# Kernel optimization log

Hardware: AMD Instinct MI355X
Metric: run time of the kernel (lower is better)

Reference implementation:

```python
import jax, jax.numpy as jnp
import numpy as np

NEG = -1e30  # safe -inf surrogate (avoids nan grads through where)
NUM_CLASSES = 128
BLANK = NUM_CLASSES - 1
B, T, L = 256, 512, 64


def setup_inputs() -> dict:
    key = jax.random.key(0)
    k1, k2, k3, k4 = jax.random.split(key, 4)
    y_pred = jax.random.normal(k1, (B, T, NUM_CLASSES), dtype=jnp.float32)
    y_true = jax.random.randint(k2, (B, L), 0, BLANK, dtype=jnp.int32)  # labels in [0, C-2]
    input_length = jax.random.randint(k3, (B,), T // 2, T + 1, dtype=jnp.int32)
    label_length = jax.random.randint(k4, (B,), L // 2, L + 1, dtype=jnp.int32)
    return {"y_true": y_true, "y_pred": y_pred,
            "input_length": input_length, "label_length": label_length}


def ctc_loss(y_pred, y_true, input_length, label_length):
    # y_pred: [B,T,C] logits (batch-major), y_true: [B,L] int labels, blank = C-1.
    Bs, Ts, C = y_pred.shape
    Ls = y_true.shape[1]
    S = 2 * Ls + 1  # extended label lattice: blank, l1, blank, l2, ..., blank
    lp = jax.nn.log_softmax(y_pred.astype(jnp.float32), axis=-1)  # [B,T,C]
    z = jnp.full((Bs, S), BLANK, dtype=jnp.int32).at[:, 1::2].set(y_true)  # [B,S]
    idx = jnp.broadcast_to(z[:, None, :], (Bs, Ts, S))
    lp_z = jnp.take_along_axis(lp, idx, axis=2)  # [B,T,S] log p(z_s | t)
    # skip transition s-2 -> s allowed when z_s is a label differing from z_{s-2}
    s_idx = jnp.arange(S)
    z_m2 = jnp.pad(z[:, :-2], ((0, 0), (2, 0)), constant_values=BLANK)
    skip = (s_idx[None, :] >= 2) & (z != BLANK) & (z != z_m2)  # [B,S]
    alpha0 = (jnp.full((Bs, S), NEG, jnp.float32)
              .at[:, 0].set(lp_z[:, 0, 0])
              .at[:, 1].set(lp_z[:, 0, 1]))
    lps = jnp.moveaxis(lp_z[:, 1:, :], 1, 0)  # [T-1, B, S]
    ts = jnp.arange(1, Ts)

    def step(alpha, xs):
        t, lpt = xs
        a1 = jnp.pad(alpha[:, :-1], ((0, 0), (1, 0)), constant_values=NEG)
        a2 = jnp.where(skip, jnp.pad(alpha[:, :-2], ((0, 0), (2, 0)), constant_values=NEG), NEG)
        new = jnp.logaddexp(jnp.logaddexp(alpha, a1), a2) + lpt
        # freeze rows whose sequence already ended (t >= input_length)
        alpha = jnp.where((t < input_length)[:, None], new, alpha)
        return alpha, None

    alphaT, _ = jax.lax.scan(step, alpha0, (ts, lps))
    e1 = (2 * label_length)[:, None]  # final blank position per row
    a_end = jnp.take_along_axis(alphaT, e1, axis=1)[:, 0]
    a_end2 = jnp.take_along_axis(alphaT, e1 - 1, axis=1)[:, 0]
    return -jnp.logaddexp(a_end, a_end2)  # [B] negative log-likelihood


def reference(y_true, y_pred, input_length, label_length):
    # tf.nn.ctc_loss(labels, logits, label_length, logit_length,
    #                logits_time_major=False, blank_index=num_classes-1)
    return ctc_loss(y_pred, y_true, input_length, label_length)
```

## Files before the change

kernel.cpp:

```cpp
#include <hip/hip_runtime.h>
#include <hip/hip_fp16.h>
#include <math.h>


constexpr int Cc = 128;
constexpr int Tt = 512;
constexpr int Ll = 64;
constexpr int NPS = 7;
constexpr float INV_LN2 = 1.4426950408889634f;
constexpr float LN2_F   = 0.6931471805599453f;
constexpr float RENORM_THR = 16777216.0f;

__device__ __forceinline__ float fexp2(float x) { return __builtin_amdgcn_exp2f(x); }
__device__ __forceinline__ float flog2(float x) { return __builtin_amdgcn_logf(x); }

template<int CTRL, bool BC>
__device__ __forceinline__ float dppf(float old, float x) {
    return __int_as_float(__builtin_amdgcn_update_dpp(
        __float_as_int(old), __float_as_int(x), CTRL, 0xF, 0xF, BC));
}
__device__ __forceinline__ float wshr1(float x, float fill) { return dppf<0x138, false>(fill, x); }
__device__ __forceinline__ float wshl1(float x, float fill) { return dppf<0x130, false>(fill, x); }

__device__ __forceinline__ float rlf(float v, int lane) {
    return __int_as_float(__builtin_amdgcn_readlane(__float_as_int(v), lane));
}
__device__ __forceinline__ float rowsum(float e) {
    e += dppf<0x111, true>(0.f, e);
    e += dppf<0x112, true>(0.f, e);
    e += dppf<0x114, true>(0.f, e);
    e += dppf<0x118, true>(0.f, e);
    return e;
}
__device__ __forceinline__ float xmax64(float m) {
    m = fmaxf(m, __shfl_xor(m, 32, 64));
    m = fmaxf(m, __shfl_xor(m, 16, 64));
    m = fmaxf(m, __shfl_xor(m,  8, 64));
    m = fmaxf(m, __shfl_xor(m,  4, 64));
    m = fmaxf(m, __shfl_xor(m,  2, 64));
    m = fmaxf(m, __shfl_xor(m,  1, 64));
    return m;
}
__device__ __forceinline__ float bperm_f(int srclane, float v) {
    return __int_as_float(__builtin_amdgcn_ds_bpermute(srclane << 2, __float_as_int(v)));
}
__device__ __forceinline__ double shflx_d(double v, int mask) {
    const long long x = __double_as_longlong(v);
    int lo = (int)(x & 0xffffffffLL), hi = (int)(x >> 32);
    lo = __shfl_xor(lo, mask, 64);
    hi = __shfl_xor(hi, mask, 64);
    return __longlong_as_double(((long long)hi << 32) | (unsigned)(unsigned int)lo);
}

__device__ __forceinline__ void unpack8(uint4 raw, float (&dv)[8]) {
    const __half2 h0 = *reinterpret_cast<const __half2*>(&raw.x);
    const __half2 h1 = *reinterpret_cast<const __half2*>(&raw.y);
    const __half2 h2 = *reinterpret_cast<const __half2*>(&raw.z);
    const __half2 h3 = *reinterpret_cast<const __half2*>(&raw.w);
    dv[0] = __low2float(h0); dv[1] = __high2float(h0);
    dv[2] = __low2float(h1); dv[3] = __high2float(h1);
    dv[4] = __low2float(h2); dv[5] = __high2float(h2);
    dv[6] = __low2float(h3); dv[7] = __high2float(h3);
}

template<bool GUARD>
__device__ __forceinline__ void do_chunk(uint4 raw, int t0, int inlen, float skf,
                                         float& aO, float& aE, float& r0, float& Rtot)
{
    float dv[8]; unpack8(raw, dv);
    float sd[8];
#pragma unroll
    for (int j = 0; j < 8; ++j) sd[j] = skf * dv[j];
#pragma unroll
    for (int j = 0; j < 8; ++j) {
        if (!GUARD || (t0 + j < inlen)) {
            const float ad = aO * dv[j];
            const float pE = wshr1(aE, r0);
            const float pO = wshr1(aO, 0.0f);
            const float nO = fmaf(pE, dv[j], fmaf(pO, sd[j], ad));
            aE += aO;
            aO = nO;
        }
    }
    const float mx = fmaxf(fmaxf(aO, aE), r0);
    if (__any(mx >= RENORM_THR)) {
        const float M_ = xmax64(mx);
        int R_ = (int)(__float_as_uint(M_) >> 23) - 127;
        R_ = (R_ < 0) ? 0 : ((R_ > 126) ? 126 : R_);
        const float sc = __uint_as_float((unsigned)(127 - R_) << 23);
        aO = fminf(aO * sc, 4.0f);
        aE = fminf(aE * sc, 4.0f);
        r0 = fminf(r0 * sc, 4.0f);
        Rtot += (float)R_;
    }
}

template<bool GUARD>
__device__ __forceinline__ void do_chunk_bwd(uint4 raw, int t0, int inlen, float skfb,
                                             float& bO, float& bE, float& br, float& Rb,
                                             int l)
{
    float dv[8]; unpack8(raw, dv);
#pragma unroll
    for (int j = 7; j >= 0; --j) {
        if (!GUARD || (t0 + j < inlen)) {
            const float BOw = bO * dv[j];
            const float uO  = wshl1(BOw, 0.0f);
            const float t1  = bE + BOw;
            bE += uO;
            br += BOw;
            bO  = fmaf(skfb, uO, t1);
        }
    }
    const float brm = (l == 0) ? br : 0.0f;
    const float mx = fmaxf(fmaxf(bO, bE), brm);
    if (__any(mx >= RENORM_THR)) {
        const float M_ = xmax64(mx);
        int R_ = (int)(__float_as_uint(M_) >> 23) - 127;
        R_ = (R_ < 0) ? 0 : ((R_ > 126) ? 126 : R_);
        const float sc = __uint_as_float((unsigned)(127 - R_) << 23);
        bO = bO * sc;
        bE = bE * sc;
        br = br * sc;
        Rb += (float)R_;
    }
}

__global__ __launch_bounds__(1024, 1) void ctc_fused9_kernel(
    const int* __restrict__ y_true,
    const float* __restrict__ y_pred,
    const int* __restrict__ in_len,
    const int* __restrict__ lab_len,
    float* __restrict__ out)
{
    __shared__ __half w_lds[Tt / 8][64][8];
    __shared__ float  ps[2 * NPS];
    __shared__ int    fctr[10], bctr[10];
    __shared__ int    bdone, pdone;
    __shared__ float  bstate[130];

    const int b   = blockIdx.x;
    const int tid = threadIdx.x;
    const int w   = tid >> 6;
    const int l   = tid & 63;

    if (tid < 10) { fctr[tid] = 0; bctr[tid] = 0; }
    if (tid == 0) { bdone = 0; pdone = 0; }
    __syncthreads();

    int inlen = in_len[b]; if (inlen < 1) inlen = 1; if (inlen > Tt) inlen = Tt;
    int LLv   = lab_len[b]; if (LLv < 1) LLv = 1; if (LLv > Ll) LLv = Ll;

    const int nct  = (inlen + 7) >> 3;
    const int nchf = nct >> 1;
    const int nchb = nct - nchf;

    const int lab = y_true[b * Ll + l] & 127;
    const float* rowbase = y_pred + (size_t)b * Tt * Cc;

    if (w >= 2) {
        const bool asc = (w < 9);
        const int pw    = asc ? (w - 2) : (w - 9);
        const int nside = asc ? nchf : nchb;
        const int glane = lab >> 1;
        const int lsel  = lab & 1;
        const bool live = (l < LLv);
        int* ctr = asc ? fctr : bctr;

        float acc = 0.0f;

        for (int k = pw, idx = 0; k < nside; k += NPS, ++idx) {
            const int c = asc ? k : (nct - 1 - k);
            const int row0 = c * 8;
            float2 rv[8];
#pragma unroll
            for (int t = 0; t < 8; ++t)
                rv[t] = ((const float2*)(rowbase + (size_t)(row0 + t) * Cc))[l];

            float prod = 1.0f, bsum = 0.0f;
            uint4 pk;

            auto wbits = [&](int t) -> unsigned {
                const float2 v = rv[t];
                float e = fexp2(v.x * INV_LN2) + fexp2(v.y * INV_LN2);
                e = rowsum(e);
                const float s  = (rlf(e, 15) + rlf(e, 31)) + (rlf(e, 47) + rlf(e, 63));
                const float bl = rlf(v.y, 63);
                const bool ok = (row0 + t) < inlen;
                prod *= ok ? s : 1.0f;
                bsum += ok ? bl : 0.0f;
                const float xa = bperm_f(glane, v.x);
                const float xb = bperm_f(glane, v.y);
                const float xl = lsel ? xb : xa;
                float ww = fminf(fmaxf(fexp2((xl - bl) * INV_LN2), 6.1e-5f), 8192.0f);
                ww = live ? ww : 0.0f;
                return (unsigned)__half_as_ushort(__float2half(ww));
            };
            pk.x = wbits(0) | (wbits(1) << 16);
            pk.y = wbits(2) | (wbits(3) << 16);
            pk.z = wbits(4) | (wbits(5) << 16);
            pk.w = wbits(6) | (wbits(7) << 16);

            acc = fmaf(bsum, INV_LN2, acc) - flog2(prod);
            *(uint4*)&w_lds[c][l][0] = pk;
            asm volatile("s_waitcnt lgkmcnt(0)" ::: "memory");
            if (l == 0) atomicAdd(&ctr[idx], 1);
        }
        if (l == 0) ps[(asc ? 0 : NPS) + pw] = acc;
        asm volatile("s_waitcnt lgkmcnt(0)" ::: "memory");
        if (l == 0) atomicAdd(&pdone, 1);
        return;
    }

    const int labp = __shfl_up(lab, 1, 64);
    const float skf = ((l >= 1) && (lab != labp)) ? 1.0f : 0.0f;

    if (w == 1) {
        const float skfb = __shfl(skf, (l + 1) & 63, 64);
        float bE = (l == LLv - 1) ? 1.0f : 0.0f;
        float bO = bE;
        float br = 0.0f, Rb = 0.0f;

        volatile int* vd = bctr;
        int readyd = 0, rrd = 0;
        auto wait_d = [&](int cb) {
            const int needcnt = nct - cb;
            while (readyd < needcnt) {
                const int rem  = nchb - rrd * NPS;
                const int need = rem < NPS ? rem : NPS;
                if (vd[rrd] >= need) { readyd += need; ++rrd; }
                else __builtin_amdgcn_s_sleep(1);
            }
            asm volatile("" ::: "memory");
        };

        if (nchb > 0) {
            wait_d(nct - 1);
            uint4 A = *(const uint4*)&w_lds[nct - 1][l][0];
            for (int cb = nct - 1; cb >= nchf; --cb) {
                uint4 Bv = A;
                if (cb - 1 >= nchf) { wait_d(cb - 1); Bv = *(const uint4*)&w_lds[cb - 1][l][0]; }
                const int t0 = cb * 8;
                if (t0 + 8 <= inlen) do_chunk_bwd<false>(A, t0, inlen, skfb, bO, bE, br, Rb, l);
                else                 do_chunk_bwd<true >(A, t0, inlen, skfb, bO, bE, br, Rb, l);
                A = Bv;
            }
        }
        bstate[l]      = bE;
        bstate[64 + l] = bO;
        if (l == 0) { bstate[128] = br; bstate[129] = Rb; }
        asm volatile("s_waitcnt lgkmcnt(0)" ::: "memory");
        if (l == 0) atomicExch(&bdone, 1);
        return;
    }

    float aO = 0.0f, aE = 0.0f, r0 = 1.0f, Rf = 0.0f;

    volatile int* vf = fctr;
    int readyf = 0, rrf = 0;
    auto wait_f = [&](int cneed) {
        while (readyf <= cneed) {
            const int rem  = nchf - rrf * NPS;
            const int need = rem < NPS ? rem : NPS;
            if (vf[rrf] >= need) { readyf += need; ++rrf; }
            else __builtin_amdgcn_s_sleep(1);
        }
        asm volatile("" ::: "memory");
    };

    if (nchf > 0) {
        wait_f(0);
        uint4 A = *(const uint4*)&w_lds[0][l][0];
        for (int c = 0; c < nchf; ++c) {
            uint4 Bv = A;
            if (c + 1 < nchf) { wait_f(c + 1); Bv = *(const uint4*)&w_lds[c + 1][l][0]; }
            const int t0 = c * 8;
            if (t0 + 8 <= inlen) do_chunk<false>(A, t0, inlen, skf, aO, aE, r0, Rf);
            else                 do_chunk<true >(A, t0, inlen, skf, aO, aE, r0, Rf);
            A = Bv;
        }
    }

    {
        volatile int* vp = &pdone;
        while (*vp < 2 * NPS) __builtin_amdgcn_s_sleep(1);
        volatile int* vbd = &bdone;
        while (*vbd == 0) __builtin_amdgcn_s_sleep(1);
        asm volatile("" ::: "memory");
    }

    float cum_b = 0.0f;
#pragma unroll
    for (int q = 0; q < 2 * NPS; ++q) cum_b += ps[q];

    const float bEl = bstate[l], bOl = bstate[64 + l];
    const float br0 = bstate[128], Rb = bstate[129];
    double cd = (double)aE * (double)bEl + (double)aO * (double)bOl;
    if (l == 0) cd += (double)r0 * (double)br0;
#pragma unroll
    for (int mk = 1; mk < 64; mk <<= 1) cd += shflx_d(cd, mk);
    double sd_ = cd > 1e-300 ? cd : 1e-300;
    const long long u = __double_as_longlong(sd_);
    const int e2 = (int)((u >> 52) & 0x7ff) - 1023;
    const double mant = __longlong_as_double((u & 0xfffffffffffffLL) | 0x3ff0000000000000LL);
    const float l2s = (float)e2 + flog2((float)mant);
    if (l == 0)
        out[b] = -LN2_F * (l2s + Rf + Rb + cum_b);
}

extern "C" void kernel_launch(void* const* d_in, const int* in_sizes, int n_in,
                              void* d_out, int out_size, void* d_ws, size_t ws_size,
                              hipStream_t stream) {
    const int*   y_true  = (const int*)d_in[0];
    const float* y_pred  = (const float*)d_in[1];
    const int*   in_len  = (const int*)d_in[2];
    const int*   lab_len = (const int*)d_in[3];
    float*       out     = (float*)d_out;
    (void)d_ws; (void)ws_size;

    ctc_fused9_kernel<<<256, 1024, 0, stream>>>(y_true, y_pred, in_len, lab_len, out);
}
```

Baseline: 108.6 us.

## Decouple recurrence waves from normalizer waves; gather label logits directly with prefetch

Before, 14 producer waves computed per-timestep label weights, stored them to LDS as fp16, and signalled two recurrence waves through spin-waited counters. Now the forward and backward waves gather their own label logits and blank logits straight from global memory through a 4-deep register prefetch ring. The other waves only compute the log-sum-exp normalizer, using a DPP row-broadcast full-wave sum instead of four readlanes. A single __syncthreads replaces the flag polling. The intent is to remove the producer-consumer latency and the LDS traffic from the serial critical path, at the cost of scattered global gathers inside the recurrence waves. The forward path also drops its per-step inlen guard, and the launch bound changes to allow 4 blocks per CU.

```diff
diff --git a/kernel.cpp b/kernel.cpp
--- a/kernel.cpp
+++ b/kernel.cpp
@@ -6,7 +6,6 @@
 constexpr int Cc = 128;
 constexpr int Tt = 512;
 constexpr int Ll = 64;
-constexpr int NPS = 7;
 constexpr float INV_LN2 = 1.4426950408889634f;
 constexpr float LN2_F   = 0.6931471805599453f;
 constexpr float RENORM_THR = 16777216.0f;
@@ -30,6 +29,12 @@
     e += dppf<0x112, true>(0.f, e);
     e += dppf<0x114, true>(0.f, e);
     e += dppf<0x118, true>(0.f, e);
+    return e;
+}
+__device__ __forceinline__ float sum64_l63(float e) {
+    e = rowsum(e);
+    e += dppf<0x142, true>(0.f, e);
+    e += dppf<0x143, true>(0.f, e);
     return e;
 }
 __device__ __forceinline__ float xmax64(float m) {
@@ -41,9 +46,6 @@
     m = fmaxf(m, __shfl_xor(m,  1, 64));
     return m;
 }
-__device__ __forceinline__ float bperm_f(int srclane, float v) {
-    return __int_as_float(__builtin_amdgcn_ds_bpermute(srclane << 2, __float_as_int(v)));
-}
 __device__ __forceinline__ double shflx_d(double v, int mask) {
     const long long x = __double_as_longlong(v);
     int lo = (int)(x & 0xffffffffLL), hi = (int)(x >> 32);
@@ -52,35 +54,20 @@
     return __longlong_as_double(((long long)hi << 32) | (unsigned)(unsigned int)lo);
 }
 
-__device__ __forceinline__ void unpack8(uint4 raw, float (&dv)[8]) {
-    const __half2 h0 = *reinterpret_cast<const __half2*>(&raw.x);
-    const __half2 h1 = *reinterpret_cast<const __half2*>(&raw.y);
-    const __half2 h2 = *reinterpret_cast<const __half2*>(&raw.z);
-    const __half2 h3 = *reinterpret_cast<const __half2*>(&raw.w);
-    dv[0] = __low2float(h0); dv[1] = __high2float(h0);
-    dv[2] = __low2float(h1); dv[3] = __high2float(h1);
-    dv[4] = __low2float(h2); dv[5] = __high2float(h2);
-    dv[6] = __low2float(h3); dv[7] = __high2float(h3);
-}
-
-template<bool GUARD>
-__device__ __forceinline__ void do_chunk(uint4 raw, int t0, int inlen, float skf,
-                                         float& aO, float& aE, float& r0, float& Rtot)
+__device__ __forceinline__ void do_chunk_f(const float (&dv)[8], float skf,
+                                           float& aO, float& aE, float& r0, float& Rtot)
 {
-    float dv[8]; unpack8(raw, dv);
     float sd[8];
 #pragma unroll
     for (int j = 0; j < 8; ++j) sd[j] = skf * dv[j];
 #pragma unroll
     for (int j = 0; j < 8; ++j) {
-        if (!GUARD || (t0 + j < inlen)) {
-            const float ad = aO * dv[j];
-            const float pE = wshr1(aE, r0);
-            const float pO = wshr1(aO, 0.0f);
-            const float nO = fmaf(pE, dv[j], fmaf(pO, sd[j], ad));
-            aE += aO;
-            aO = nO;
-        }
+        const float ad = aO * dv[j];
+        const float pE = wshr1(aE, r0);
+        const float pO = wshr1(aO, 0.0f);
+        const float nO = fmaf(pE, dv[j], fmaf(pO, sd[j], ad));
+        aE += aO;
+        aO = nO;
     }
     const float mx = fmaxf(fmaxf(aO, aE), r0);
     if (__any(mx >= RENORM_THR)) {
@@ -96,11 +83,10 @@
 }
 
 template<bool GUARD>
-__device__ __forceinline__ void do_chunk_bwd(uint4 raw, int t0, int inlen, float skfb,
-                                             float& bO, float& bE, float& br, float& Rb,
-                                             int l)
+__device__ __forceinline__ void do_chunk_b(const float (&dv)[8], int t0, int inlen,
+                                           float skfb, float& bO, float& bE,
+                                           float& br, float& Rb, int l)
 {
-    float dv[8]; unpack8(raw, dv);
 #pragma unroll
     for (int j = 7; j >= 0; --j) {
         if (!GUARD || (t0 + j < inlen)) {
@@ -126,28 +112,21 @@
     }
 }
 
-__global__ __launch_bounds__(1024, 1) void ctc_fused9_kernel(
+__global__ __launch_bounds__(1024, 4) void ctc_fused11_kernel(
     const int* __restrict__ y_true,
     const float* __restrict__ y_pred,
     const int* __restrict__ in_len,
     const int* __restrict__ lab_len,
     float* __restrict__ out)
 {
-    __shared__ __half w_lds[Tt / 8][64][8];
-    __shared__ float  ps[2 * NPS];
-    __shared__ int    fctr[10], bctr[10];
-    __shared__ int    bdone, pdone;
-    __shared__ float  bstate[130];
+    __shared__ float ps[14];
+    __shared__ float bstate[130];
 
     const int b   = blockIdx.x;
     const int tid = threadIdx.x;
     const int w   = tid >> 6;
     const int l   = tid & 63;
 
-    if (tid < 10) { fctr[tid] = 0; bctr[tid] = 0; }
-    if (tid == 0) { bdone = 0; pdone = 0; }
-    __syncthreads();
-
     int inlen = in_len[b]; if (inlen < 1) inlen = 1; if (inlen > Tt) inlen = Tt;
     int LLv   = lab_len[b]; if (LLv < 1) LLv = 1; if (LLv > Ll) LLv = Ll;
 
@@ -158,154 +137,143 @@
     const int lab = y_true[b * Ll + l] & 127;
     const float* rowbase = y_pred + (size_t)b * Tt * Cc;
 
+    const int labp = __shfl_up(lab, 1, 64);
+    const float skf = ((l >= 1) && (lab != labp)) ? 1.0f : 0.0f;
+    const bool live = (l < LLv);
+
     if (w >= 2) {
-        const bool asc = (w < 9);
-        const int pw    = asc ? (w - 2) : (w - 9);
-        const int nside = asc ? nchf : nchb;
-        const int glane = lab >> 1;
-        const int lsel  = lab & 1;
-        const bool live = (l < LLv);
-        int* ctr = asc ? fctr : bctr;
-
+        const int wv = w - 2;
         float acc = 0.0f;
-
-        for (int k = pw, idx = 0; k < nside; k += NPS, ++idx) {
-            const int c = asc ? k : (nct - 1 - k);
-            const int row0 = c * 8;
-            float2 rv[8];
-#pragma unroll
-            for (int t = 0; t < 8; ++t)
-                rv[t] = ((const float2*)(rowbase + (size_t)(row0 + t) * Cc))[l];
-
+        float2 A[4], Bb[4];
+        auto loadg = [&](int g, float2 (&buf)[4]) {
+#pragma unroll
+            for (int q = 0; q < 4; ++q) {
+                const int r  = wv * 4 + q + 56 * g;
+                const int rc = (r < inlen) ? r : 0;
+                buf[q] = ((const float2*)(rowbase + (size_t)rc * Cc))[l];
+            }
+        };
+        auto procg = [&](int g, float2 (&buf)[4]) {
             float prod = 1.0f, bsum = 0.0f;
-            uint4 pk;
-
-            auto wbits = [&](int t) -> unsigned {
-                const float2 v = rv[t];
+#pragma unroll
+            for (int q = 0; q < 4; ++q) {
+                const float2 v = buf[q];
+                {
+                    const int r  = wv * 4 + q + 56 * (g + 2);
+                    const int rc = (r < inlen) ? r : 0;
+                    buf[q] = ((const float2*)(rowbase + (size_t)rc * Cc))[l];
+                }
+                const int r = wv * 4 + q + 56 * g;
                 float e = fexp2(v.x * INV_LN2) + fexp2(v.y * INV_LN2);
-                e = rowsum(e);
-                const float s  = (rlf(e, 15) + rlf(e, 31)) + (rlf(e, 47) + rlf(e, 63));
+                e = sum64_l63(e);
+                const float s  = rlf(e, 63);
                 const float bl = rlf(v.y, 63);
-                const bool ok = (row0 + t) < inlen;
+                const bool ok = r < inlen;
                 prod *= ok ? s : 1.0f;
                 bsum += ok ? bl : 0.0f;
-                const float xa = bperm_f(glane, v.x);
-                const float xb = bperm_f(glane, v.y);
-                const float xl = lsel ? xb : xa;
-                float ww = fminf(fmaxf(fexp2((xl - bl) * INV_LN2), 6.1e-5f), 8192.0f);
-                ww = live ? ww : 0.0f;
-                return (unsigned)__half_as_ushort(__float2half(ww));
-            };
-            pk.x = wbits(0) | (wbits(1) << 16);
-            pk.y = wbits(2) | (wbits(3) << 16);
-            pk.z = wbits(4) | (wbits(5) << 16);
-            pk.w = wbits(6) | (wbits(7) << 16);
-
+            }
             acc = fmaf(bsum, INV_LN2, acc) - flog2(prod);
-            *(uint4*)&w_lds[c][l][0] = pk;
-            asm volatile("s_waitcnt lgkmcnt(0)" ::: "memory");
-            if (l == 0) atomicAdd(&ctr[idx], 1);
-        }
-        if (l == 0) ps[(asc ? 0 : NPS) + pw] = acc;
-        asm volatile("s_waitcnt lgkmcnt(0)" ::: "memory");
-        if (l == 0) atomicAdd(&pdone, 1);
-        return;
-    }
-
-    const int labp = __shfl_up(lab, 1, 64);
-    const float skf = ((l >= 1) && (lab != labp)) ? 1.0f : 0.0f;
-
-    if (w == 1) {
+        };
+        loadg(0, A); loadg(1, Bb);
+        for (int g = 0; g < 10; g += 2) { procg(g, A); procg(g + 1, Bb); }
+        if (l == 0) ps[wv] = acc;
+    } else if (w == 1) {
         const float skfb = __shfl(skf, (l + 1) & 63, 64);
         float bE = (l == LLv - 1) ? 1.0f : 0.0f;
         float bO = bE;
         float br = 0.0f, Rb = 0.0f;
-
-        volatile int* vd = bctr;
-        int readyd = 0, rrd = 0;
-        auto wait_d = [&](int cb) {
-            const int needcnt = nct - cb;
-            while (readyd < needcnt) {
-                const int rem  = nchb - rrd * NPS;
-                const int need = rem < NPS ? rem : NPS;
-                if (vd[rrd] >= need) { readyd += need; ++rrd; }
-                else __builtin_amdgcn_s_sleep(1);
-            }
-            asm volatile("" ::: "memory");
-        };
-
-        if (nchb > 0) {
-            wait_d(nct - 1);
-            uint4 A = *(const uint4*)&w_lds[nct - 1][l][0];
-            for (int cb = nct - 1; cb >= nchf; --cb) {
-                uint4 Bv = A;
-                if (cb - 1 >= nchf) { wait_d(cb - 1); Bv = *(const uint4*)&w_lds[cb - 1][l][0]; }
-                const int t0 = cb * 8;
-                if (t0 + 8 <= inlen) do_chunk_bwd<false>(A, t0, inlen, skfb, bO, bE, br, Rb, l);
-                else                 do_chunk_bwd<true >(A, t0, inlen, skfb, bO, bE, br, Rb, l);
-                A = Bv;
-            }
+        const int nch = nchb;
+
+        float X0[8], X1[8], X2[8], X3[8];
+        float V0, V1, V2, V3;
+        auto issue = [&](int k, float (&X)[8], float& BV) {
+            const int cc = (k < nch) ? k : (nch - 1);
+            const int row0 = (nct - 1 - cc) * 8;
+#pragma unroll
+            for (int j = 0; j < 8; ++j)
+                X[j] = rowbase[(size_t)(row0 + j) * Cc + lab];
+            BV = rowbase[(size_t)(row0 + (l & 7)) * Cc + 127];
+        };
+        auto compute = [&](int k, float (&X)[8], float& BV) {
+            if (k >= nch) return;
+            float dv[8];
+#pragma unroll
+            for (int j = 0; j < 8; ++j) {
+                const float bl = __shfl(BV, j, 64);
+                const float ww = fminf(fmaxf(fexp2((X[j] - bl) * INV_LN2),
+                                             6.1e-5f), 8192.0f);
+                dv[j] = live ? ww : 0.0f;
+            }
+            const int t0 = (nct - 1 - k) * 8;
+            if (t0 + 8 <= inlen) do_chunk_b<false>(dv, t0, inlen, skfb, bO, bE, br, Rb, l);
+            else                 do_chunk_b<true >(dv, t0, inlen, skfb, bO, bE, br, Rb, l);
+        };
+        issue(0, X0, V0); issue(1, X1, V1); issue(2, X2, V2);
+        for (int k = 0; k < nch; k += 4) {
+            issue(k + 3, X3, V3); compute(k + 0, X0, V0);
+            issue(k + 4, X0, V0); compute(k + 1, X1, V1);
+            issue(k + 5, X1, V1); compute(k + 2, X2, V2);
+            issue(k + 6, X2, V2); compute(k + 3, X3, V3);
         }
         bstate[l]      = bE;
         bstate[64 + l] = bO;
         if (l == 0) { bstate[128] = br; bstate[129] = Rb; }
-        asm volatile("s_waitcnt lgkmcnt(0)" ::: "memory");
-        if (l == 0) atomicExch(&bdone, 1);
-        return;
-    }
-
+    }
     float aO = 0.0f, aE = 0.0f, r0 = 1.0f, Rf = 0.0f;
-
-    volatile int* vf = fctr;
-    int readyf = 0, rrf = 0;
-    auto wait_f = [&](int cneed) {
-        while (readyf <= cneed) {
-            const int rem  = nchf - rrf * NPS;
-            const int need = rem < NPS ? rem : NPS;
-            if (vf[rrf] >= need) { readyf += need; ++rrf; }
-            else __builtin_amdgcn_s_sleep(1);
+    if (w == 0) {
+        const int nch = nchf;
+        float X0[8], X1[8], X2[8], X3[8];
+        float V0, V1, V2, V3;
+        auto issue = [&](int k, float (&X)[8], float& BV) {
+            const int cc = (k < nch) ? k : (nch - 1);
+            const int row0 = cc * 8;
+#pragma unroll
+            for (int j = 0; j < 8; ++j)
+                X[j] = rowbase[(size_t)(row0 + j) * Cc + lab];
+            BV = rowbase[(size_t)(row0 + (l & 7)) * Cc + 127];
+        };
+        auto compute = [&](int k, float (&X)[8], float& BV) {
+            if (k >= nch) return;
+            float dv[8];
+#pragma unroll
+            for (int j = 0; j < 8; ++j) {
+                const float bl = __shfl(BV, j, 64);
+                const float ww = fminf(fmaxf(fexp2((X[j] - bl) * INV_LN2),
+                                             6.1e-5f), 8192.0f);
+                dv[j] = live ? ww : 0.0f;
+            }
+            do_chunk_f(dv, skf, aO, aE, r0, Rf);
+        };
+        issue(0, X0, V0); issue(1, X1, V1); issue(2, X2, V2);
+        for (int k = 0; k < nch; k += 4) {
+            issue(k + 3, X3, V3); compute(k + 0, X0, V0);
+            issue(k + 4, X0, V0); compute(k + 1, X1, V1);
+            issue(k + 5, X1, V1); compute(k + 2, X2, V2);
+            issue(k + 6, X2, V2); compute(k + 3, X3, V3);
         }
-        asm volatile("" ::: "memory");
-    };
-
-    if (nchf > 0) {
-        wait_f(0);
-        uint4 A = *(const uint4*)&w_lds[0][l][0];
-        for (int c = 0; c < nchf; ++c) {
-            uint4 Bv = A;
-            if (c + 1 < nchf) { wait_f(c + 1); Bv = *(const uint4*)&w_lds[c + 1][l][0]; }
-            const int t0 = c * 8;
-            if (t0 + 8 <= inlen) do_chunk<false>(A, t0, inlen, skf, aO, aE, r0, Rf);
-            else                 do_chunk<true >(A, t0, inlen, skf, aO, aE, r0, Rf);
-            A = Bv;
-        }
-    }
-
-    {
-        volatile int* vp = &pdone;
-        while (*vp < 2 * NPS) __builtin_amdgcn_s_sleep(1);
-        volatile int* vbd = &bdone;
-        while (*vbd == 0) __builtin_amdgcn_s_sleep(1);
-        asm volatile("" ::: "memory");
-    }
-
-    float cum_b = 0.0f;
-#pragma unroll
-    for (int q = 0; q < 2 * NPS; ++q) cum_b += ps[q];
-
-    const float bEl = bstate[l], bOl = bstate[64 + l];
-    const float br0 = bstate[128], Rb = bstate[129];
-    double cd = (double)aE * (double)bEl + (double)aO * (double)bOl;
-    if (l == 0) cd += (double)r0 * (double)br0;
-#pragma unroll
-    for (int mk = 1; mk < 64; mk <<= 1) cd += shflx_d(cd, mk);
-    double sd_ = cd > 1e-300 ? cd : 1e-300;
-    const long long u = __double_as_longlong(sd_);
-    const int e2 = (int)((u >> 52) & 0x7ff) - 1023;
-    const double mant = __longlong_as_double((u & 0xfffffffffffffLL) | 0x3ff0000000000000LL);
-    const float l2s = (float)e2 + flog2((float)mant);
-    if (l == 0)
-        out[b] = -LN2_F * (l2s + Rf + Rb + cum_b);
+    }
+
+    __syncthreads();
+
+    if (w == 0) {
+        float cum_b = 0.0f;
+#pragma unroll
+        for (int q = 0; q < 14; ++q) cum_b += ps[q];
+
+        const float bEl = bstate[l], bOl = bstate[64 + l];
+        const float br0 = bstate[128], Rb = bstate[129];
+        double cd = (double)aE * (double)bEl + (double)aO * (double)bOl;
+        if (l == 0) cd += (double)r0 * (double)br0;
+#pragma unroll
+        for (int mk = 1; mk < 64; mk <<= 1) cd += shflx_d(cd, mk);
+        double sd_ = cd > 1e-300 ? cd : 1e-300;
+        const long long u = __double_as_longlong(sd_);
+        const int e2 = (int)((u >> 52) & 0x7ff) - 1023;
+        const double mant = __longlong_as_double((u & 0xfffffffffffffLL) | 0x3ff0000000000000LL);
+        const float l2s = (float)e2 + flog2((float)mant);
+        if (l == 0)
+            out[b] = -LN2_F * (l2s + Rf + Rb + cum_b);
+    }
 }
 
 extern "C" void kernel_launch(void* const* d_in, const int* in_sizes, int n_in,
@@ -318,5 +286,5 @@
     float*       out     = (float*)d_out;
     (void)d_ws; (void)ws_size;
 
-    ctc_fused9_kernel<<<256, 1024, 0, stream>>>(y_true, y_pred, in_len, lab_len, out);
-}
+    ctc_fused11_kernel<<<256, 1024, 0, stream>>>(y_true, y_pred, in_len, lab_len, out);
+}
```

Result: slower. 114.9 us (+5.8%).

## Split forward and backward CTC passes into separate blocks with combine kernel

Applied to the files above, without the earlier changes.

Launches two blocks per batch row, one running the forward alpha recursion and one the backward beta recursion, each with 15 producer waves computing emission weights into LDS. A small second kernel combines the two halves' states from workspace memory into the final loss. This is meant to double block-level parallelism and give each serial recursion more producer waves. In exchange it adds a second launch and a global-memory round trip, and it keeps the old single-block kernel as a fallback when no workspace is available.

```diff
diff --git a/kernel.cpp b/kernel.cpp
--- a/kernel.cpp
+++ b/kernel.cpp
@@ -6,10 +6,10 @@
 constexpr int Cc = 128;
 constexpr int Tt = 512;
 constexpr int Ll = 64;
-constexpr int NPS = 7;
 constexpr float INV_LN2 = 1.4426950408889634f;
 constexpr float LN2_F   = 0.6931471805599453f;
 constexpr float RENORM_THR = 16777216.0f;
+constexpr int PAYSTRIDE = 132;
 
 __device__ __forceinline__ float fexp2(float x) { return __builtin_amdgcn_exp2f(x); }
 __device__ __forceinline__ float flog2(float x) { return __builtin_amdgcn_logf(x); }
@@ -63,9 +63,8 @@
     dv[6] = __low2float(h3); dv[7] = __high2float(h3);
 }
 
-template<bool GUARD>
-__device__ __forceinline__ void do_chunk(uint4 raw, int t0, int inlen, float skf,
-                                         float& aO, float& aE, float& r0, float& Rtot)
+__device__ __forceinline__ void do_chunk_f(uint4 raw, float skf,
+                                           float& aO, float& aE, float& r0, float& Rtot)
 {
     float dv[8]; unpack8(raw, dv);
     float sd[8];
@@ -73,14 +72,12 @@
     for (int j = 0; j < 8; ++j) sd[j] = skf * dv[j];
 #pragma unroll
     for (int j = 0; j < 8; ++j) {
-        if (!GUARD || (t0 + j < inlen)) {
-            const float ad = aO * dv[j];
-            const float pE = wshr1(aE, r0);
-            const float pO = wshr1(aO, 0.0f);
-            const float nO = fmaf(pE, dv[j], fmaf(pO, sd[j], ad));
-            aE += aO;
-            aO = nO;
-        }
+        const float ad = aO * dv[j];
+        const float pE = wshr1(aE, r0);
+        const float pO = wshr1(aO, 0.0f);
+        const float nO = fmaf(pE, dv[j], fmaf(pO, sd[j], ad));
+        aE += aO;
+        aO = nO;
     }
     const float mx = fmaxf(fmaxf(aO, aE), r0);
     if (__any(mx >= RENORM_THR)) {
@@ -96,9 +93,9 @@
 }
 
 template<bool GUARD>
-__device__ __forceinline__ void do_chunk_bwd(uint4 raw, int t0, int inlen, float skfb,
-                                             float& bO, float& bE, float& br, float& Rb,
-                                             int l)
+__device__ __forceinline__ void do_chunk_b(uint4 raw, int t0, int inlen, float skfb,
+                                           float& bO, float& bE, float& br, float& Rb,
+                                           int l)
 {
     float dv[8]; unpack8(raw, dv);
 #pragma unroll
@@ -126,51 +123,53 @@
     }
 }
 
-__global__ __launch_bounds__(1024, 1) void ctc_fused9_kernel(
+__global__ __launch_bounds__(1024, 8) void ctc_half_kernel(
     const int* __restrict__ y_true,
     const float* __restrict__ y_pred,
     const int* __restrict__ in_len,
     const int* __restrict__ lab_len,
-    float* __restrict__ out)
+    float* __restrict__ pay)
 {
-    __shared__ __half w_lds[Tt / 8][64][8];
-    __shared__ float  ps[2 * NPS];
-    __shared__ int    fctr[10], bctr[10];
-    __shared__ int    bdone, pdone;
-    __shared__ float  bstate[130];
-
-    const int b   = blockIdx.x;
+    constexpr int NPSH = 15;
+    constexpr int NRDH = 3;
+    __shared__ __half w_lds[32][64][8];
+    __shared__ float  ps[NPSH];
+    __shared__ int    ctr[NRDH];
+
+    const int dir = blockIdx.x & 1;
+    const int b   = blockIdx.x >> 1;
     const int tid = threadIdx.x;
     const int w   = tid >> 6;
     const int l   = tid & 63;
 
-    if (tid < 10) { fctr[tid] = 0; bctr[tid] = 0; }
-    if (tid == 0) { bdone = 0; pdone = 0; }
+    if (tid < NRDH) ctr[tid] = 0;
     __syncthreads();
 
     int inlen = in_len[b]; if (inlen < 1) inlen = 1; if (inlen > Tt) inlen = Tt;
     int LLv   = lab_len[b]; if (LLv < 1) LLv = 1; if (LLv > Ll) LLv = Ll;
 
-    const int nct  = (inlen + 7) >> 3;
-    const int nchf = nct >> 1;
-    const int nchb = nct - nchf;
+    const int nct   = (inlen + 7) >> 3;
+    const int nchf  = nct >> 1;
+    const int nchb  = nct - nchf;
+    const int nside = dir ? nchb : nchf;
 
     const int lab = y_true[b * Ll + l] & 127;
     const float* rowbase = y_pred + (size_t)b * Tt * Cc;
 
-    if (w >= 2) {
-        const bool asc = (w < 9);
-        const int pw    = asc ? (w - 2) : (w - 9);
-        const int nside = asc ? nchf : nchb;
+    const int labp = __shfl_up(lab, 1, 64);
+    const float skf = ((l >= 1) && (lab != labp)) ? 1.0f : 0.0f;
+    const bool live = (l < LLv);
+
+    float stE = 0.0f, stO = 0.0f, stX = 0.0f, stR = 0.0f;
+
+    if (w >= 1) {
+        const int pw = w - 1;
         const int glane = lab >> 1;
         const int lsel  = lab & 1;
-        const bool live = (l < LLv);
-        int* ctr = asc ? fctr : bctr;
-
         float acc = 0.0f;
 
-        for (int k = pw, idx = 0; k < nside; k += NPS, ++idx) {
-            const int c = asc ? k : (nct - 1 - k);
+        for (int k = pw, idx = 0; k < nside; k += NPSH, ++idx) {
+            const int c = dir ? (nct - 1 - k) : k;
             const int row0 = c * 8;
             float2 rv[8];
 #pragma unroll
@@ -179,7 +178,6 @@
 
             float prod = 1.0f, bsum = 0.0f;
             uint4 pk;
-
             auto wbits = [&](int t) -> unsigned {
                 const float2 v = rv[t];
                 float e = fexp2(v.x * INV_LN2) + fexp2(v.y * INV_LN2);
@@ -202,6 +200,167 @@
             pk.w = wbits(6) | (wbits(7) << 16);
 
             acc = fmaf(bsum, INV_LN2, acc) - flog2(prod);
+            *(uint4*)&w_lds[k][l][0] = pk;
+            asm volatile("s_waitcnt lgkmcnt(0)" ::: "memory");
+            if (l == 0) atomicAdd(&ctr[idx], 1);
+        }
+        if (l == 0) ps[pw] = acc;
+    } else {
+        volatile int* vc = ctr;
+        int ready = 0, rr = 0;
+        auto wait_k = [&](int kneed) {
+            while (ready <= kneed) {
+                const int rem  = nside - rr * NPSH;
+                const int need = rem < NPSH ? rem : NPSH;
+                if (vc[rr] >= need) { ready += need; ++rr; }
+                else __builtin_amdgcn_s_sleep(1);
+            }
+            asm volatile("" ::: "memory");
+        };
+
+        if (dir == 0) {
+            float aO = 0.0f, aE = 0.0f, r0 = 1.0f, Rf = 0.0f;
+            if (nside > 0) {
+                wait_k(0);
+                uint4 A = *(const uint4*)&w_lds[0][l][0];
+                for (int k = 0; k < nside; ++k) {
+                    uint4 Bv = A;
+                    if (k + 1 < nside) { wait_k(k + 1); Bv = *(const uint4*)&w_lds[k + 1][l][0]; }
+                    do_chunk_f(A, skf, aO, aE, r0, Rf);
+                    A = Bv;
+                }
+            }
+            stE = aE; stO = aO; stX = r0; stR = Rf;
+        } else {
+            const float skfb = __shfl(skf, (l + 1) & 63, 64);
+            float bE = (l == LLv - 1) ? 1.0f : 0.0f;
+            float bO = bE;
+            float br = 0.0f, Rb = 0.0f;
+            if (nside > 0) {
+                wait_k(0);
+                uint4 A = *(const uint4*)&w_lds[0][l][0];
+                for (int k = 0; k < nside; ++k) {
+                    uint4 Bv = A;
+                    if (k + 1 < nside) { wait_k(k + 1); Bv = *(const uint4*)&w_lds[k + 1][l][0]; }
+                    const int t0 = (nct - 1 - k) * 8;
+                    if (t0 + 8 <= inlen) do_chunk_b<false>(A, t0, inlen, skfb, bO, bE, br, Rb, l);
+                    else                 do_chunk_b<true >(A, t0, inlen, skfb, bO, bE, br, Rb, l);
+                    A = Bv;
+                }
+            }
+            stE = bE; stO = bO; stX = br; stR = Rb;
+        }
+    }
+
+    __syncthreads();
+
+    if (w == 0) {
+        float cumb = 0.0f;
+#pragma unroll
+        for (int q = 0; q < NPSH; ++q) cumb += ps[q];
+        float* mine = pay + (size_t)(b * 2 + dir) * PAYSTRIDE;
+        mine[l]      = stE;
+        mine[64 + l] = stO;
+        if (l == 0) { mine[128] = stX; mine[129] = stR; mine[130] = cumb; }
+    }
+}
+
+__global__ void ctc_combine_kernel(const float* __restrict__ pay,
+                                   float* __restrict__ out)
+{
+    const int b = blockIdx.x;
+    const int l = threadIdx.x;
+    const float* fs = pay + (size_t)(b * 2 + 0) * PAYSTRIDE;
+    const float* bs = pay + (size_t)(b * 2 + 1) * PAYSTRIDE;
+    const float aE = fs[l], aO = fs[64 + l];
+    const float r0 = fs[128], Rf = fs[129], cbf = fs[130];
+    const float bE = bs[l], bO = bs[64 + l];
+    const float br = bs[128], Rb = bs[129], cbb = bs[130];
+
+    double cd = (double)aE * (double)bE + (double)aO * (double)bO;
+    if (l == 0) cd += (double)r0 * (double)br;
+#pragma unroll
+    for (int mk = 1; mk < 64; mk <<= 1) cd += shflx_d(cd, mk);
+    double sd_ = cd > 1e-300 ? cd : 1e-300;
+    const long long u = __double_as_longlong(sd_);
+    const int e2 = (int)((u >> 52) & 0x7ff) - 1023;
+    const double mant = __longlong_as_double((u & 0xfffffffffffffLL) | 0x3ff0000000000000LL);
+    const float l2s = (float)e2 + flog2((float)mant);
+    if (l == 0)
+        out[b] = -LN2_F * (l2s + Rf + Rb + cbf + cbb);
+}
+
+__global__ __launch_bounds__(1024, 1) void ctc_fb_kernel(
+    const int* __restrict__ y_true, const float* __restrict__ y_pred,
+    const int* __restrict__ in_len, const int* __restrict__ lab_len,
+    float* __restrict__ out)
+{
+    constexpr int NPS = 7;
+    __shared__ __half w_lds[Tt / 8][64][8];
+    __shared__ float  ps[2 * NPS];
+    __shared__ int    fctr[10], bctr[10];
+    __shared__ int    bdone, pdone;
+    __shared__ float  bstate[130];
+
+    const int b   = blockIdx.x;
+    const int tid = threadIdx.x;
+    const int w   = tid >> 6;
+    const int l   = tid & 63;
+
+    if (tid < 10) { fctr[tid] = 0; bctr[tid] = 0; }
+    if (tid == 0) { bdone = 0; pdone = 0; }
+    __syncthreads();
+
+    int inlen = in_len[b]; if (inlen < 1) inlen = 1; if (inlen > Tt) inlen = Tt;
+    int LLv   = lab_len[b]; if (LLv < 1) LLv = 1; if (LLv > Ll) LLv = Ll;
+
+    const int nct  = (inlen + 7) >> 3;
+    const int nchf = nct >> 1;
+    const int nchb = nct - nchf;
+
+    const int lab = y_true[b * Ll + l] & 127;
+    const float* rowbase = y_pred + (size_t)b * Tt * Cc;
+
+    if (w >= 2) {
+        const bool asc = (w < 9);
+        const int pw    = asc ? (w - 2) : (w - 9);
+        const int nside = asc ? nchf : nchb;
+        const int glane = lab >> 1;
+        const int lsel  = lab & 1;
+        const bool live = (l < LLv);
+        int* ctr = asc ? fctr : bctr;
+        float acc = 0.0f;
+
+        for (int k = pw, idx = 0; k < nside; k += NPS, ++idx) {
+            const int c = asc ? k : (nct - 1 - k);
+            const int row0 = c * 8;
+            float2 rv[8];
+#pragma unroll
+            for (int t = 0; t < 8; ++t)
+                rv[t] = ((const float2*)(rowbase + (size_t)(row0 + t) * Cc))[l];
+            float prod = 1.0f, bsum = 0.0f;
+            uint4 pk;
+            auto wbits = [&](int t) -> unsigned {
+                const float2 v = rv[t];
+                float e = fexp2(v.x * INV_LN2) + fexp2(v.y * INV_LN2);
+                e = rowsum(e);
+                const float s  = (rlf(e, 15) + rlf(e, 31)) + (rlf(e, 47) + rlf(e, 63));
+                const float bl = rlf(v.y, 63);
+                const bool ok = (row0 + t) < inlen;
+                prod *= ok ? s : 1.0f;
+                bsum += ok ? bl : 0.0f;
+                const float xa = bperm_f(glane, v.x);
+                const float xb = bperm_f(glane, v.y);
+                const float xl = lsel ? xb : xa;
+                float ww = fminf(fmaxf(fexp2((xl - bl) * INV_LN2), 6.1e-5f), 8192.0f);
+                ww = live ? ww : 0.0f;
+                return (unsigned)__half_as_ushort(__float2half(ww));
+            };
+            pk.x = wbits(0) | (wbits(1) << 16);
+            pk.y = wbits(2) | (wbits(3) << 16);
+            pk.z = wbits(4) | (wbits(5) << 16);
+            pk.w = wbits(6) | (wbits(7) << 16);
+            acc = fmaf(bsum, INV_LN2, acc) - flog2(prod);
             *(uint4*)&w_lds[c][l][0] = pk;
             asm volatile("s_waitcnt lgkmcnt(0)" ::: "memory");
             if (l == 0) atomicAdd(&ctr[idx], 1);
@@ -220,7 +379,6 @@
         float bE = (l == LLv - 1) ? 1.0f : 0.0f;
         float bO = bE;
         float br = 0.0f, Rb = 0.0f;
-
         volatile int* vd = bctr;
         int readyd = 0, rrd = 0;
         auto wait_d = [&](int cb) {
@@ -233,7 +391,6 @@
             }
             asm volatile("" ::: "memory");
         };
-
         if (nchb > 0) {
             wait_d(nct - 1);
             uint4 A = *(const uint4*)&w_lds[nct - 1][l][0];
@@ -241,8 +398,8 @@
                 uint4 Bv = A;
                 if (cb - 1 >= nchf) { wait_d(cb - 1); Bv = *(const uint4*)&w_lds[cb - 1][l][0]; }
                 const int t0 = cb * 8;
-                if (t0 + 8 <= inlen) do_chunk_bwd<false>(A, t0, inlen, skfb, bO, bE, br, Rb, l);
-                else                 do_chunk_bwd<true >(A, t0, inlen, skfb, bO, bE, br, Rb, l);
+                if (t0 + 8 <= inlen) do_chunk_b<false>(A, t0, inlen, skfb, bO, bE, br, Rb, l);
+                else                 do_chunk_b<true >(A, t0, inlen, skfb, bO, bE, br, Rb, l);
                 A = Bv;
             }
         }
@@ -255,7 +412,6 @@
     }
 
     float aO = 0.0f, aE = 0.0f, r0 = 1.0f, Rf = 0.0f;
-
     volatile int* vf = fctr;
     int readyf = 0, rrf = 0;
     auto wait_f = [&](int cneed) {
@@ -267,20 +423,16 @@
         }
         asm volatile("" ::: "memory");
     };
-
     if (nchf > 0) {
         wait_f(0);
         uint4 A = *(const uint4*)&w_lds[0][l][0];
         for (int c = 0; c < nchf; ++c) {
             uint4 Bv = A;
             if (c + 1 < nchf) { wait_f(c + 1); Bv = *(const uint4*)&w_lds[c + 1][l][0]; }
-            const int t0 = c * 8;
-            if (t0 + 8 <= inlen) do_chunk<false>(A, t0, inlen, skf, aO, aE, r0, Rf);
-            else                 do_chunk<true >(A, t0, inlen, skf, aO, aE, r0, Rf);
+            do_chunk_f(A, skf, aO, aE, r0, Rf);
             A = Bv;
         }
     }
-
     {
         volatile int* vp = &pdone;
         while (*vp < 2 * NPS) __builtin_amdgcn_s_sleep(1);
@@ -288,11 +440,9 @@
         while (*vbd == 0) __builtin_amdgcn_s_sleep(1);
         asm volatile("" ::: "memory");
     }
-
     float cum_b = 0.0f;
 #pragma unroll
     for (int q = 0; q < 2 * NPS; ++q) cum_b += ps[q];
-
     const float bEl = bstate[l], bOl = bstate[64 + l];
     const float br0 = bstate[128], Rb = bstate[129];
     double cd = (double)aE * (double)bEl + (double)aO * (double)bOl;
@@ -316,7 +466,13 @@
     const int*   in_len  = (const int*)d_in[2];
     const int*   lab_len = (const int*)d_in[3];
     float*       out     = (float*)d_out;
-    (void)d_ws; (void)ws_size;
-
-    ctc_fused9_kernel<<<256, 1024, 0, stream>>>(y_true, y_pred, in_len, lab_len, out);
-}
+
+    const size_t need = (size_t)256 * 2 * PAYSTRIDE * sizeof(float);
+    if (d_ws != nullptr && ws_size >= need) {
+        float* pay = (float*)d_ws;
+        ctc_half_kernel<<<512, 1024, 0, stream>>>(y_true, y_pred, in_len, lab_len, pay);
+        ctc_combine_kernel<<<256, 64, 0, stream>>>(pay, out);
+    } else {
+        ctc_fb_kernel<<<256, 1024, 0, stream>>>(y_true, y_pred, in_len, lab_len, out);
+    }
+}
```

After: 114.3 us. 5.2% more time.
